# Kernel tuning notes

Measured on AMD Instinct MI355X. Metric: run time of the kernel, lower is better.

Reference implementation:

```python
import jax, jax.numpy as jnp
import numpy as np

IN, OUT = 8192, 8192
MAX_STATES = 100
THRESHOLD = float(MAX_STATES // 2)  # 50


def setup_inputs() -> dict:
    key = jax.random.key(0)
    k1, k2, k3, k4, k5 = jax.random.split(key, 5)
    states = jax.random.normal(k1, (OUT, IN), dtype=jnp.float32) * 2.0 + (THRESHOLD - 2.0)
    mask = jax.random.uniform(k2, (OUT, IN)) < 0.1
    states = jnp.clip(jnp.where(mask, states + 5.0, states), 1.0, float(MAX_STATES))
    spike_input = (jax.random.uniform(k3, (IN,)) < 0.5).astype(jnp.float32)
    v_mem = jnp.zeros((OUT,), dtype=jnp.float32)
    v_th = jnp.full((OUT,), 2.0, dtype=jnp.float32)
    elig = jnp.zeros((OUT, IN), dtype=jnp.float32)
    noise = jax.random.normal(k5, (OUT,), dtype=jnp.float32) * 0.05  # thermal noise
    return {"spike_input": spike_input, "states": states, "v_mem": v_mem,
            "v_th": v_th, "elig": elig, "noise": noise}


def reference(spike_input, states, v_mem, v_th, elig, noise):
    # ternary weights from synapse states (0/1 mask)
    w = (states > THRESHOLD).astype(jnp.float32)          # [O, I]
    current = w @ spike_input                              # [O]  GEMV
    v_new = v_mem * 0.8 + current + noise                  # membrane decay + drive
    spikes = (v_new >= v_th).astype(jnp.float32)           # [O]
    # eligibility trace: decay + outer(post, pre), clamp
    elig_new = jnp.clip(elig * 0.95 + jnp.outer(spikes, spike_input), 0.0, 5.0)
    # adaptive threshold homeostasis
    v_th_new = jnp.clip(v_th + (spikes - 0.05) * 0.1, 0.5, 10.0)
    # soft reset of membrane where spiked
    v_mem_new = v_new * (1.0 - spikes) * 0.2
    return spikes, v_mem_new, v_th_new, elig_new
```

## Files before the change

### kernel.cpp

```cpp
#include <hip/hip_runtime.h>

#define SNN_IN  8192
#define SNN_OUT 8192
#define SNN_THRESHOLD 50.0f

__global__ __launch_bounds__(256) void snn_fused_kernel(
    const float* __restrict__ spike_in,
    const float* __restrict__ states,
    const float* __restrict__ v_mem,
    const float* __restrict__ v_th,
    const float* __restrict__ elig,
    const float* __restrict__ noise,
    float* __restrict__ out_spikes,
    float* __restrict__ out_vmem,
    float* __restrict__ out_vth,
    float* __restrict__ out_elig)
{
    const int row = blockIdx.x;
    const int tid = threadIdx.x;
    const size_t row_off4 = (size_t)row * (SNN_IN / 4);

    const float4* __restrict__ s4  = reinterpret_cast<const float4*>(states) + row_off4;
    const float4* __restrict__ sp4 = reinterpret_cast<const float4*>(spike_in);

    float partial = 0.0f;
    #pragma unroll
    for (int p = 0; p < SNN_IN / 4 / 256; ++p) {
        const int idx = p * 256 + tid;
        const float4 s  = s4[idx];
        const float4 sp = sp4[idx];
        partial += (s.x > SNN_THRESHOLD ? sp.x : 0.0f)
                 + (s.y > SNN_THRESHOLD ? sp.y : 0.0f)
                 + (s.z > SNN_THRESHOLD ? sp.z : 0.0f)
                 + (s.w > SNN_THRESHOLD ? sp.w : 0.0f);
    }

    #pragma unroll
    for (int off = 32; off > 0; off >>= 1)
        partial += __shfl_down(partial, off, 64);

    __shared__ float wsum[4];
    __shared__ float s_spike;
    const int wave = tid >> 6;
    if ((tid & 63) == 0) wsum[wave] = partial;
    __syncthreads();

    if (tid == 0) {
        const float current = wsum[0] + wsum[1] + wsum[2] + wsum[3];
        const float v_new = v_mem[row] * 0.8f + current + noise[row];
        const float spike = (v_new >= v_th[row]) ? 1.0f : 0.0f;
        out_spikes[row] = spike;
        out_vmem[row]   = v_new * (1.0f - spike) * 0.2f;
        const float vt  = v_th[row] + (spike - 0.05f) * 0.1f;
        out_vth[row]    = fminf(fmaxf(vt, 0.5f), 10.0f);
        s_spike = spike;
    }
    __syncthreads();
    const float spike = s_spike;

    const float4* __restrict__ e4 = reinterpret_cast<const float4*>(elig) + row_off4;
    float4* __restrict__ o4       = reinterpret_cast<float4*>(out_elig) + row_off4;
    #pragma unroll
    for (int p = 0; p < SNN_IN / 4 / 256; ++p) {
        const int idx = p * 256 + tid;
        const float4 e  = e4[idx];
        const float4 sp = sp4[idx];
        float4 r;
        r.x = fminf(fmaxf(fmaf(e.x, 0.95f, spike * sp.x), 0.0f), 5.0f);
        r.y = fminf(fmaxf(fmaf(e.y, 0.95f, spike * sp.y), 0.0f), 5.0f);
        r.z = fminf(fmaxf(fmaf(e.z, 0.95f, spike * sp.z), 0.0f), 5.0f);
        r.w = fminf(fmaxf(fmaf(e.w, 0.95f, spike * sp.w), 0.0f), 5.0f);
        o4[idx] = r;
    }
}

extern "C" void kernel_launch(void* const* d_in, const int* in_sizes, int n_in,
                              void* d_out, int out_size, void* d_ws, size_t ws_size,
                              hipStream_t stream) {
    const float* spike_in = (const float*)d_in[0];
    const float* states   = (const float*)d_in[1];
    const float* v_mem    = (const float*)d_in[2];
    const float* v_th     = (const float*)d_in[3];
    const float* elig     = (const float*)d_in[4];
    const float* noise    = (const float*)d_in[5];

    float* out            = (float*)d_out;
    float* out_spikes     = out;
    float* out_vmem       = out + SNN_OUT;
    float* out_vth        = out + 2 * SNN_OUT;
    float* out_elig       = out + 3 * SNN_OUT;

    snn_fused_kernel<<<SNN_OUT, 256, 0, stream>>>(
        spike_in, states, v_mem, v_th, elig, noise,
        out_spikes, out_vmem, out_vth, out_elig);
}
```

Measured before the change: 583.2 us.

## Prefetch eligibility rows before reduction and drop second block barrier

```diff
diff --git a/kernel.cpp b/kernel.cpp
--- a/kernel.cpp
+++ b/kernel.cpp
@@ -2,9 +2,11 @@
 
 #define SNN_IN  8192
 #define SNN_OUT 8192
-#define SNN_THRESHOLD 50.0f
+#define SNN_THR 50.0f
+#define BLK     512
+#define VPT     (SNN_IN / 4 / BLK)
 
-__global__ __launch_bounds__(256) void snn_fused_kernel(
+__global__ __launch_bounds__(BLK) void snn_fused_kernel(
     const float* __restrict__ spike_in,
     const float* __restrict__ states,
     const float* __restrict__ v_mem,
@@ -18,58 +20,69 @@
 {
     const int row = blockIdx.x;
     const int tid = threadIdx.x;
-    const size_t row_off4 = (size_t)row * (SNN_IN / 4);
+    const size_t row4 = (size_t)row * (SNN_IN / 4);
 
-    const float4* __restrict__ s4  = reinterpret_cast<const float4*>(states) + row_off4;
+    const float4* __restrict__ s4  = reinterpret_cast<const float4*>(states) + row4;
+    const float4* __restrict__ e4  = reinterpret_cast<const float4*>(elig)   + row4;
     const float4* __restrict__ sp4 = reinterpret_cast<const float4*>(spike_in);
+
+    const float vm = v_mem[row];
+    const float vt = v_th[row];
+    const float nz = noise[row];
+
+    float4 s[VPT], e[VPT], sp[VPT];
+    #pragma unroll
+    for (int j = 0; j < VPT; ++j) {
+        const int idx = j * BLK + tid;
+        sp[j] = sp4[idx];
+        s[j]  = s4[idx];
+        e[j]  = e4[idx];
+    }
 
     float partial = 0.0f;
     #pragma unroll
-    for (int p = 0; p < SNN_IN / 4 / 256; ++p) {
-        const int idx = p * 256 + tid;
-        const float4 s  = s4[idx];
-        const float4 sp = sp4[idx];
-        partial += (s.x > SNN_THRESHOLD ? sp.x : 0.0f)
-                 + (s.y > SNN_THRESHOLD ? sp.y : 0.0f)
-                 + (s.z > SNN_THRESHOLD ? sp.z : 0.0f)
-                 + (s.w > SNN_THRESHOLD ? sp.w : 0.0f);
+    for (int j = 0; j < VPT; ++j) {
+        partial += (s[j].x > SNN_THR ? sp[j].x : 0.0f)
+                 + (s[j].y > SNN_THR ? sp[j].y : 0.0f)
+                 + (s[j].z > SNN_THR ? sp[j].z : 0.0f)
+                 + (s[j].w > SNN_THR ? sp[j].w : 0.0f);
     }
 
     #pragma unroll
     for (int off = 32; off > 0; off >>= 1)
         partial += __shfl_down(partial, off, 64);
 
-    __shared__ float wsum[4];
-    __shared__ float s_spike;
-    const int wave = tid >> 6;
-    if ((tid & 63) == 0) wsum[wave] = partial;
+    __shared__ float wsum[BLK / 64];
+    if ((tid & 63) == 0) wsum[tid >> 6] = partial;
+
+    #pragma unroll
+    for (int j = 0; j < VPT; ++j)
+        asm volatile("" :: "v"(e[j].x), "v"(e[j].y), "v"(e[j].z), "v"(e[j].w));
+
     __syncthreads();
 
+    float total = 0.0f;
+    #pragma unroll
+    for (int w = 0; w < BLK / 64; ++w) total += wsum[w];
+
+    const float v_new = vm * 0.8f + total + nz;
+    const float spike = (v_new >= vt) ? 1.0f : 0.0f;
+
     if (tid == 0) {
-        const float current = wsum[0] + wsum[1] + wsum[2] + wsum[3];
-        const float v_new = v_mem[row] * 0.8f + current + noise[row];
-        const float spike = (v_new >= v_th[row]) ? 1.0f : 0.0f;
         out_spikes[row] = spike;
         out_vmem[row]   = v_new * (1.0f - spike) * 0.2f;
-        const float vt  = v_th[row] + (spike - 0.05f) * 0.1f;
-        out_vth[row]    = fminf(fmaxf(vt, 0.5f), 10.0f);
-        s_spike = spike;
+        out_vth[row]    = fminf(fmaxf(vt + (spike - 0.05f) * 0.1f, 0.5f), 10.0f);
     }
-    __syncthreads();
-    const float spike = s_spike;
 
-    const float4* __restrict__ e4 = reinterpret_cast<const float4*>(elig) + row_off4;
-    float4* __restrict__ o4       = reinterpret_cast<float4*>(out_elig) + row_off4;
+    float4* __restrict__ o4 = reinterpret_cast<float4*>(out_elig) + row4;
     #pragma unroll
-    for (int p = 0; p < SNN_IN / 4 / 256; ++p) {
-        const int idx = p * 256 + tid;
-        const float4 e  = e4[idx];
-        const float4 sp = sp4[idx];
+    for (int j = 0; j < VPT; ++j) {
+        const int idx = j * BLK + tid;
         float4 r;
-        r.x = fminf(fmaxf(fmaf(e.x, 0.95f, spike * sp.x), 0.0f), 5.0f);
-        r.y = fminf(fmaxf(fmaf(e.y, 0.95f, spike * sp.y), 0.0f), 5.0f);
-        r.z = fminf(fmaxf(fmaf(e.z, 0.95f, spike * sp.z), 0.0f), 5.0f);
-        r.w = fminf(fmaxf(fmaf(e.w, 0.95f, spike * sp.w), 0.0f), 5.0f);
+        r.x = fminf(fmaxf(fmaf(e[j].x, 0.95f, spike * sp[j].x), 0.0f), 5.0f);
+        r.y = fminf(fmaxf(fmaf(e[j].y, 0.95f, spike * sp[j].y), 0.0f), 5.0f);
+        r.z = fminf(fmaxf(fmaf(e[j].z, 0.95f, spike * sp[j].z), 0.0f), 5.0f);
+        r.w = fminf(fmaxf(fmaf(e[j].w, 0.95f, spike * sp[j].w), 0.0f), 5.0f);
         o4[idx] = r;
     }
 }
@@ -84,13 +97,13 @@
     const float* elig     = (const float*)d_in[4];
     const float* noise    = (const float*)d_in[5];
 
-    float* out            = (float*)d_out;
-    float* out_spikes     = out;
-    float* out_vmem       = out + SNN_OUT;
-    float* out_vth        = out + 2 * SNN_OUT;
-    float* out_elig       = out + 3 * SNN_OUT;
+    float* out        = (float*)d_out;
+    float* out_spikes = out;
+    float* out_vmem   = out + SNN_OUT;
+    float* out_vth    = out + 2 * SNN_OUT;
+    float* out_elig   = out + 3 * SNN_OUT;
 
-    snn_fused_kernel<<<SNN_OUT, 256, 0, stream>>>(
+    snn_fused_kernel<<<SNN_OUT, BLK, 0, stream>>>(
         spike_in, states, v_mem, v_th, elig, noise,
         out_spikes, out_vmem, out_vth, out_elig);
 }
```

New measurement: 586.3 us. No clear change (+0.5%).
